# Performance work log

Measured on AMD Instinct MI355X. Metric: run time of the kernel, lower is better.

The kernel has to match this reference:

```python
import jax, jax.numpy as jnp
import numpy as np
import math

DIM = 1024
HEADS = 16
B, N = 2, 2048

POLY = jnp.array([-0.037, 0.481, -2.3, 4.917, -1.791], dtype=jnp.float32)


def adaptive_temperature_softmax(logits):
    # logits: [b, h, n, n]
    original_probs = jax.nn.softmax(logits, axis=-1)
    entropy = jnp.sum(-original_probs * jnp.log(original_probs + 1e-9), axis=-1, keepdims=True)
    e2 = entropy * entropy
    poly_result = POLY[0] * e2 * e2 + POLY[1] * e2 * entropy + POLY[2] * e2 + POLY[3] * entropy + POLY[4]
    beta = jnp.where(entropy > 0.5, jnp.maximum(poly_result, 1.0), 1.0)
    return jax.nn.softmax(logits * beta, axis=-1)


def setup_inputs() -> dict:
    key = jax.random.key(0)
    ks = jax.random.split(key, 5)
    s = 1.0 / math.sqrt(DIM)
    return {
        "x": jax.random.normal(ks[0], (B, N, DIM), dtype=jnp.float32),
        "Wq": jax.random.normal(ks[1], (DIM, DIM), dtype=jnp.float32) * s,
        "Wk": jax.random.normal(ks[2], (DIM, DIM), dtype=jnp.float32) * s,
        "Wv": jax.random.normal(ks[3], (DIM, DIM), dtype=jnp.float32) * s,
        "Wo": jax.random.normal(ks[4], (DIM, DIM), dtype=jnp.float32) * s,
        "bo": jnp.zeros((DIM,), dtype=jnp.float32),
    }


def reference(x, Wq, Wk, Wv, Wo, bo):
    b, n, d = x.shape
    h = HEADS
    hd = d // h
    # torch nn.Linear: y = x @ W.T (+ bias)
    def proj(W):
        t = x @ W.T  # [b, n, d]
        return t.reshape(b, n, h, hd).transpose(0, 2, 1, 3)  # [b, h, n, hd]
    q, k, v = proj(Wq), proj(Wk), proj(Wv)
    sim = jnp.einsum('bhid,bhjd->bhij', q, k) / math.sqrt(hd)
    neg = -jnp.finfo(sim.dtype).max
    causal = jnp.triu(jnp.ones((n, n), dtype=bool), k=1)  # True above diagonal
    sim = jnp.where(causal, neg, sim)
    attn = adaptive_temperature_softmax(sim)
    out = jnp.einsum('bhij,bhjd->bhid', attn, v)
    out = out.transpose(0, 2, 1, 3).reshape(b, n, d)
    return out @ Wo.T + bo
```

## Files before the change

### kernel.cpp

```cpp
#include <hip/hip_runtime.h>
#include <math.h>

#define B_   2
#define N_   2048
#define D_   1024
#define H_   16
#define HD_  64
#define BH_  32
#define M_   4096

typedef __bf16 bf16x8 __attribute__((ext_vector_type(8)));
typedef float  f32x4  __attribute__((ext_vector_type(4)));

__device__ inline unsigned short f2b(float f) {
    unsigned u = __float_as_uint(f);
    u += 0x7FFFu + ((u >> 16) & 1u);
    return (unsigned short)(u >> 16);
}
__device__ inline unsigned short f2b_fast(float f) {
    return (unsigned short)((__float_as_uint(f) + 0x8000u) >> 16);
}

__global__ __launch_bounds__(256)
void cvt_all(const float* __restrict__ x,  const float* __restrict__ wq,
             const float* __restrict__ wk, const float* __restrict__ wv,
             const float* __restrict__ wo, ushort* __restrict__ dst)
{
    int i = blockIdx.x * 256 + threadIdx.x;
    if (i >= 2097152) return;
    int fi = i * 4;
    const float* s; int off;
    if (fi < 4194304) { s = x; off = fi; }
    else {
        int r = fi - 4194304;
        int wsel = r >> 20;
        off = r & 1048575;
        s = (wsel == 0) ? wq : (wsel == 1) ? wk : (wsel == 2) ? wv : wo;
    }
    float4 f = *(const float4*)(s + off);
    ushort4 o;
    o.x = f2b(f.x); o.y = f2b(f.y); o.z = f2b(f.z); o.w = f2b(f.w);
    *(ushort4*)(dst + fi) = o;
}

__global__ __launch_bounds__(256)
void gemm_qkv(const ushort* __restrict__ A,
              const ushort* __restrict__ W0, const ushort* __restrict__ W1,
              const ushort* __restrict__ W2,
              ushort* __restrict__ O0, ushort* __restrict__ O1,
              ushort* __restrict__ O2)
{
    const int z = blockIdx.z;
    const ushort* W = (z == 0) ? W0 : (z == 1) ? W1 : W2;

    __shared__ alignas(16) ushort As[128][40];
    __shared__ alignas(16) ushort Bs[128][40];

    const int t = threadIdx.x;
    const int lane = t & 63, w = t >> 6;
    const int quad = lane >> 4, l15 = lane & 15;
    const int wm = (w >> 1) * 64, wn = (w & 1) * 64;
    const int tileM = blockIdx.x * 128, tileN = blockIdx.y * 128;

    const int r0 = t >> 2, r1 = 64 + (t >> 2);
    const int cg = (t & 3) * 8;
    const ushort* GA0 = A + (size_t)(tileM + r0) * D_ + cg;
    const ushort* GA1 = A + (size_t)(tileM + r1) * D_ + cg;
    const ushort* GB0 = W + (size_t)(tileN + r0) * D_ + cg;
    const ushort* GB1 = W + (size_t)(tileN + r1) * D_ + cg;

    f32x4 acc[4][4];
#pragma unroll
    for (int mt = 0; mt < 4; ++mt)
#pragma unroll
        for (int nt = 0; nt < 4; ++nt) acc[mt][nt] = (f32x4){0.f, 0.f, 0.f, 0.f};

    uint4 pa0 = *(const uint4*)GA0, pa1 = *(const uint4*)GA1;
    uint4 pb0 = *(const uint4*)GB0, pb1 = *(const uint4*)GB1;

    for (int k0 = 0; k0 < D_; k0 += 32) {
        __syncthreads();
        *(uint4*)&As[r0][cg] = pa0;
        *(uint4*)&As[r1][cg] = pa1;
        *(uint4*)&Bs[r0][cg] = pb0;
        *(uint4*)&Bs[r1][cg] = pb1;
        __syncthreads();
        if (k0 + 32 < D_) {
            pa0 = *(const uint4*)(GA0 + k0 + 32);
            pa1 = *(const uint4*)(GA1 + k0 + 32);
            pb0 = *(const uint4*)(GB0 + k0 + 32);
            pb1 = *(const uint4*)(GB1 + k0 + 32);
        }

        bf16x8 af[4], bf[4];
#pragma unroll
        for (int mt = 0; mt < 4; ++mt) af[mt] = *(const bf16x8*)&As[wm + mt * 16 + l15][quad * 8];
#pragma unroll
        for (int nt = 0; nt < 4; ++nt) bf[nt] = *(const bf16x8*)&Bs[wn + nt * 16 + l15][quad * 8];
#pragma unroll
        for (int mt = 0; mt < 4; ++mt)
#pragma unroll
            for (int nt = 0; nt < 4; ++nt)
                acc[mt][nt] = __builtin_amdgcn_mfma_f32_16x16x32_bf16(af[mt], bf[nt], acc[mt][nt], 0, 0, 0);
    }

    ushort* O = (z == 0) ? O0 : (z == 1) ? O1 : O2;
    const float scl = (z == 0) ? 0.18033688f : 1.0f;
#pragma unroll
    for (int mt = 0; mt < 4; ++mt)
#pragma unroll
        for (int nt = 0; nt < 4; ++nt) {
            if (z == 2) {
                int rg0 = tileM + wm + mt * 16 + quad * 4;
                int cgc = tileN + wn + nt * 16 + l15;
                int b = rg0 >> 11, n0 = rg0 & (N_ - 1);
                int h = cgc >> 6, dd = cgc & 63;
                ushort4 o4;
                o4.x = f2b(acc[mt][nt][0]); o4.y = f2b(acc[mt][nt][1]);
                o4.z = f2b(acc[mt][nt][2]); o4.w = f2b(acc[mt][nt][3]);
                *(ushort4*)&O[((size_t)((b * H_ + h) * HD_ + dd)) * N_ + n0] = o4;
            } else {
#pragma unroll
                for (int r = 0; r < 4; ++r) {
                    int rg = tileM + wm + mt * 16 + quad * 4 + r;
                    int cgc = tileN + wn + nt * 16 + l15;
                    int b = rg >> 11, n = rg & (N_ - 1);
                    int h = cgc >> 6, dd = cgc & 63;
                    O[(((size_t)(b * H_ + h)) * N_ + n) * HD_ + dd] = f2b(acc[mt][nt][r] * scl);
                }
            }
        }
}

__global__ __launch_bounds__(256)
void gemm_fin(const ushort* __restrict__ A, const ushort* __restrict__ W,
              const float* __restrict__ bias, float* __restrict__ Of)
{
    __shared__ alignas(16) ushort As[128][40];
    __shared__ alignas(16) ushort Bs[64][40];

    const int t = threadIdx.x;
    const int lane = t & 63, w = t >> 6;
    const int quad = lane >> 4, l15 = lane & 15;
    const int wm = (w >> 1) * 64, wn = (w & 1) * 32;
    const int tileM = blockIdx.x * 128, tileN = blockIdx.y * 64;

    const int r0 = t >> 2, r1 = 64 + (t >> 2);
    const int cg = (t & 3) * 8;
    const ushort* GA0 = A + (size_t)(tileM + r0) * D_ + cg;
    const ushort* GA1 = A + (size_t)(tileM + r1) * D_ + cg;
    const ushort* GB0 = W + (size_t)(tileN + r0) * D_ + cg;

    f32x4 acc[4][2];
#pragma unroll
    for (int mt = 0; mt < 4; ++mt)
#pragma unroll
        for (int nt = 0; nt < 2; ++nt) acc[mt][nt] = (f32x4){0.f, 0.f, 0.f, 0.f};

    uint4 pa0 = *(const uint4*)GA0, pa1 = *(const uint4*)GA1;
    uint4 pb0 = *(const uint4*)GB0;

    for (int k0 = 0; k0 < D_; k0 += 32) {
        __syncthreads();
        *(uint4*)&As[r0][cg] = pa0;
        *(uint4*)&As[r1][cg] = pa1;
        *(uint4*)&Bs[r0 & 63][cg] = pb0;
        __syncthreads();
        if (k0 + 32 < D_) {
            pa0 = *(const uint4*)(GA0 + k0 + 32);
            pa1 = *(const uint4*)(GA1 + k0 + 32);
            pb0 = *(const uint4*)(GB0 + k0 + 32);
        }

        bf16x8 af[4], bf[2];
#pragma unroll
        for (int mt = 0; mt < 4; ++mt) af[mt] = *(const bf16x8*)&As[wm + mt * 16 + l15][quad * 8];
#pragma unroll
        for (int nt = 0; nt < 2; ++nt) bf[nt] = *(const bf16x8*)&Bs[wn + nt * 16 + l15][quad * 8];
#pragma unroll
        for (int mt = 0; mt < 4; ++mt)
#pragma unroll
            for (int nt = 0; nt < 2; ++nt)
                acc[mt][nt] = __builtin_amdgcn_mfma_f32_16x16x32_bf16(af[mt], bf[nt], acc[mt][nt], 0, 0, 0);
    }

#pragma unroll
    for (int mt = 0; mt < 4; ++mt)
#pragma unroll
        for (int nt = 0; nt < 2; ++nt)
#pragma unroll
            for (int r = 0; r < 4; ++r) {
                int rg = tileM + wm + mt * 16 + quad * 4 + r;
                int cgc = tileN + wn + nt * 16 + l15;
                Of[(size_t)rg * D_ + cgc] = acc[mt][nt][r] + bias[cgc];
            }
}

__global__ __launch_bounds__(256)
void attn_mfma(const ushort* __restrict__ Q, const ushort* __restrict__ K,
               const ushort* __restrict__ VT, ushort* __restrict__ AO)
{
    const int bid = blockIdx.x;
    const int qt = 31 - (bid >> 5);
    const int bh = bid & 31;
    const size_t kvbase = (size_t)bh * N_ * HD_;

    __shared__ alignas(16) ushort Ks[128][72];
    __shared__ alignas(16) ushort Vs[64][136];
    __shared__ alignas(16) ushort Ps[4][4][296];

    const int t = threadIdx.x;
    const int lane = t & 63, w = t >> 6;
    const int quad = lane >> 4, l15 = lane & 15;
    const float SH2 = 11.5416913f;
    const float LN2 = 0.69314718f;

    const int skey = t >> 3;
    const int skc  = (t & 7) * 8;
    const ushort* KS = K + kvbase + (size_t)skey * HD_ + skc;
    const int vhd = t >> 4;
    const int vkc = (t & 15) * 8;
    const ushort* VS = VT + kvbase + (size_t)vhd * N_ + vkc;

    const int qrow = w * 16 + quad * 4;
    const int qglob = qt * 64 + qrow;
    const int b = bh >> 4, h = bh & 15;
    const int nCh = (qt + 2) >> 1;

    bf16x8 aq0, aq1;
    {
        const size_t qr = kvbase + (size_t)(qt * 64 + w * 16 + l15) * HD_;
        aq0 = *(const bf16x8*)&Q[qr + quad * 8];
        aq1 = *(const bf16x8*)&Q[qr + 32 + quad * 8];
    }

    float ez[4] = {0.f, 0.f, 0.f, 0.f};
    float sz[4] = {0.f, 0.f, 0.f, 0.f};

    uint4 k0 = *(const uint4*)KS;
    uint4 k1 = *(const uint4*)(KS + 32 * HD_);
    uint4 k2 = *(const uint4*)(KS + 64 * HD_);
    uint4 k3 = *(const uint4*)(KS + 96 * HD_);
    for (int c = 0; c < nCh; ++c) {
        __syncthreads();
        *(uint4*)&Ks[skey][skc]      = k0;
        *(uint4*)&Ks[32 + skey][skc] = k1;
        *(uint4*)&Ks[64 + skey][skc] = k2;
        *(uint4*)&Ks[96 + skey][skc] = k3;
        __syncthreads();
        if (c + 1 < nCh) {
            const ushort* nb = KS + (size_t)(c + 1) * (128 * HD_);
            k0 = *(const uint4*)nb;
            k1 = *(const uint4*)(nb + 32 * HD_);
            k2 = *(const uint4*)(nb + 64 * HD_);
            k3 = *(const uint4*)(nb + 96 * HD_);
        }
        if (c + 1 < nCh) {
#pragma unroll
            for (int nt = 0; nt < 8; ++nt) {
                f32x4 sv = (f32x4){0.f, 0.f, 0.f, 0.f};
                sv = __builtin_amdgcn_mfma_f32_16x16x32_bf16(aq0, *(const bf16x8*)&Ks[nt * 16 + l15][quad * 8], sv, 0, 0, 0);
                sv = __builtin_amdgcn_mfma_f32_16x16x32_bf16(aq1, *(const bf16x8*)&Ks[nt * 16 + l15][32 + quad * 8], sv, 0, 0, 0);
#pragma unroll
                for (int r = 0; r < 4; ++r) {
                    float sh = sv[r] - SH2;
                    float e = __builtin_amdgcn_exp2f(sh);
                    ez[r] += e;
                    sz[r] = fmaf(e, sh, sz[r]);
                }
            }
        } else {
            const int tiles = (((qt + 1) * 64) - c * 128) >> 4;
            const int kb0 = c * 128;
            for (int nt = 0; nt < tiles; ++nt) {
                f32x4 sv = (f32x4){0.f, 0.f, 0.f, 0.f};
                sv = __builtin_amdgcn_mfma_f32_16x16x32_bf16(aq0, *(const bf16x8*)&Ks[nt * 16 + l15][quad * 8], sv, 0, 0, 0);
                sv = __builtin_amdgcn_mfma_f32_16x16x32_bf16(aq1, *(const bf16x8*)&Ks[nt * 16 + l15][32 + quad * 8], sv, 0, 0, 0);
                const int kcol = kb0 + nt * 16 + l15;
#pragma unroll
                for (int r = 0; r < 4; ++r) {
                    float sh = sv[r] - SH2;
                    float e = (kcol <= qglob + r) ? __builtin_amdgcn_exp2f(sh) : 0.f;
                    ez[r] += e;
                    sz[r] = fmaf(e, sh, sz[r]);
                }
            }
        }
    }
#pragma unroll
    for (int r = 0; r < 4; ++r) {
#pragma unroll
        for (int off = 1; off < 16; off <<= 1) {
            ez[r] += __shfl_xor(ez[r], off);
            sz[r] += __shfl_xor(sz[r], off);
        }
    }

    float nbs[4], bl[4];
#pragma unroll
    for (int r = 0; r < 4; ++r) {
        float Z = ez[r];
        float Hh = LN2 * (__builtin_amdgcn_logf(Z) - sz[r] / Z);
        float bb = 1.f;
        if (Hh > 0.5f) {
            float e2 = Hh * Hh;
            float pp = -0.037f * e2 * e2 + 0.481f * e2 * Hh - 2.3f * e2 + 4.917f * Hh - 1.791f;
            bb = fmaxf(pp, 1.f);
        }
        bl[r] = bb;
        nbs[r] = -bb * SH2;
    }

    f32x4 ov[4];
#pragma unroll
    for (int nt = 0; nt < 4; ++nt) ov[nt] = (f32x4){0.f, 0.f, 0.f, 0.f};
    float zp[4] = {0.f, 0.f, 0.f, 0.f};

    k0 = *(const uint4*)KS;
    k1 = *(const uint4*)(KS + 32 * HD_);
    k2 = *(const uint4*)(KS + 64 * HD_);
    k3 = *(const uint4*)(KS + 96 * HD_);
    uint4 v0 = *(const uint4*)VS;
    uint4 v1 = *(const uint4*)(VS + 16 * N_);
    uint4 v2 = *(const uint4*)(VS + 32 * N_);
    uint4 v3 = *(const uint4*)(VS + 48 * N_);
    for (int c = 0; c < nCh; ++c) {
        __syncthreads();
        *(uint4*)&Ks[skey][skc]      = k0;
        *(uint4*)&Ks[32 + skey][skc] = k1;
        *(uint4*)&Ks[64 + skey][skc] = k2;
        *(uint4*)&Ks[96 + skey][skc] = k3;
        *(uint4*)&Vs[vhd][vkc]       = v0;
        *(uint4*)&Vs[16 + vhd][vkc]  = v1;
        *(uint4*)&Vs[32 + vhd][vkc]  = v2;
        *(uint4*)&Vs[48 + vhd][vkc]  = v3;
        __syncthreads();
        if (c + 1 < nCh) {
            const ushort* nk = KS + (size_t)(c + 1) * (128 * HD_);
            k0 = *(const uint4*)nk;
            k1 = *(const uint4*)(nk + 32 * HD_);
            k2 = *(const uint4*)(nk + 64 * HD_);
            k3 = *(const uint4*)(nk + 96 * HD_);
            const ushort* nv = VS + (c + 1) * 128;
            v0 = *(const uint4*)nv;
            v1 = *(const uint4*)(nv + 16 * N_);
            v2 = *(const uint4*)(nv + 32 * N_);
            v3 = *(const uint4*)(nv + 48 * N_);
        }
        const int halves = min(2, (qt + 1) - c * 2);
        for (int hh = 0; hh < halves; ++hh) {
            const bool diag = (c * 2 + hh == qt);

            float wv[4][4];
#pragma unroll
            for (int nt = 0; nt < 4; ++nt) {
                f32x4 sv = (f32x4){0.f, 0.f, 0.f, 0.f};
                sv = __builtin_amdgcn_mfma_f32_16x16x32_bf16(aq0, *(const bf16x8*)&Ks[hh * 64 + nt * 16 + l15][quad * 8], sv, 0, 0, 0);
                sv = __builtin_amdgcn_mfma_f32_16x16x32_bf16(aq1, *(const bf16x8*)&Ks[hh * 64 + nt * 16 + l15][32 + quad * 8], sv, 0, 0, 0);
                const int kcol = nt * 16 + l15;
#pragma unroll
                for (int r = 0; r < 4; ++r) {
                    float e = __builtin_amdgcn_exp2f(fmaf(bl[r], sv[r], nbs[r]));
                    wv[nt][r] = (!diag || (kcol <= qrow + r)) ? e : 0.f;
                }
            }
#pragma unroll
            for (int nt = 0; nt < 4; ++nt)
#pragma unroll
                for (int r = 0; r < 4; ++r)
                    Ps[w][quad][r * 72 + nt * 16 + l15] = f2b_fast(wv[nt][r]);
#pragma unroll
            for (int r = 0; r < 4; ++r)
                zp[r] += (wv[0][r] + wv[1][r]) + (wv[2][r] + wv[3][r]);

            bf16x8 pa0 = *(const bf16x8*)&Ps[w][l15 >> 2][(l15 & 3) * 72 + quad * 8];
            bf16x8 pa1 = *(const bf16x8*)&Ps[w][l15 >> 2][(l15 & 3) * 72 + 32 + quad * 8];
#pragma unroll
            for (int nt = 0; nt < 4; ++nt) {
                ov[nt] = __builtin_amdgcn_mfma_f32_16x16x32_bf16(pa0, *(const bf16x8*)&Vs[nt * 16 + l15][hh * 64 + quad * 8], ov[nt], 0, 0, 0);
                ov[nt] = __builtin_amdgcn_mfma_f32_16x16x32_bf16(pa1, *(const bf16x8*)&Vs[nt * 16 + l15][hh * 64 + 32 + quad * 8], ov[nt], 0, 0, 0);
            }
        }
    }
#pragma unroll
    for (int r = 0; r < 4; ++r)
#pragma unroll
        for (int off = 1; off < 16; off <<= 1) zp[r] += __shfl_xor(zp[r], off);

#pragma unroll
    for (int r = 0; r < 4; ++r) {
        int qg = qt * 64 + w * 16 + quad * 4 + r;
        float inv = 1.f / zp[r];
        size_t rowoff = ((size_t)(b * N_ + qg)) * D_ + h * HD_;
#pragma unroll
        for (int nt = 0; nt < 4; ++nt)
            AO[rowoff + nt * 16 + l15] = f2b(ov[nt][r] * inv);
    }
}

extern "C" void kernel_launch(void* const* d_in, const int* in_sizes, int n_in,
                              void* d_out, int out_size, void* d_ws, size_t ws_size,
                              hipStream_t stream)
{
    const float* x  = (const float*)d_in[0];
    const float* Wq = (const float*)d_in[1];
    const float* Wk = (const float*)d_in[2];
    const float* Wv = (const float*)d_in[3];
    const float* Wo = (const float*)d_in[4];
    const float* bo = (const float*)d_in[5];
    float* out = (float*)d_out;

    ushort* ws  = (ushort*)d_ws;
    ushort* xb  = ws;
    ushort* wqb = ws + 4194304;
    ushort* wkb = ws + 5242880;
    ushort* wvb = ws + 6291456;
    ushort* wob = ws + 7340032;
    ushort* Qb  = ws + 8388608;
    ushort* Kb  = ws + 12582912;
    ushort* Vtb = ws + 16777216;
    ushort* aob = ws + 20971520;

    cvt_all<<<8192, 256, 0, stream>>>(x, Wq, Wk, Wv, Wo, xb);

    gemm_qkv<<<dim3(32, 8, 3), 256, 0, stream>>>(
        xb, wqb, wkb, wvb, Qb, Kb, Vtb);

    attn_mfma<<<dim3(1024), 256, 0, stream>>>(Qb, Kb, Vtb, aob);

    gemm_fin<<<dim3(32, 16), 256, 0, stream>>>(aob, wob, bo, out);
}
```

Measured before the change: 202.0 us.

## Load GEMM tiles directly into LDS and fold softmax shift into MFMA accumulator

The QKV and output-projection GEMMs now use global_load_lds to copy tiles straight from global memory into unpadded shared memory. This replaces the register-staged prefetch and the LDS store step, but it drops the one-step prefetch overlap and the padding that avoided bank conflicts. In the attention kernel, the constant softmax shift is now the initial value of the MFMA accumulator, which removes a subtraction per score. The second pass computes exp2(beta*(s-SH2)) with a multiply instead of an fma with a precomputed offset; the result is mathematically equivalent.

```diff
diff --git a/kernel.cpp b/kernel.cpp
--- a/kernel.cpp
+++ b/kernel.cpp
@@ -11,6 +11,11 @@
 
 typedef __bf16 bf16x8 __attribute__((ext_vector_type(8)));
 typedef float  f32x4  __attribute__((ext_vector_type(4)));
+
+#define AS1_ __attribute__((address_space(1)))
+#define AS3_ __attribute__((address_space(3)))
+#define GLDS16(g, l) __builtin_amdgcn_global_load_lds( \
+    (const AS1_ void*)(g), (AS3_ void*)(l), 16, 0, 0)
 
 __device__ inline unsigned short f2b(float f) {
     unsigned u = __float_as_uint(f);
@@ -53,8 +58,8 @@
     const int z = blockIdx.z;
     const ushort* W = (z == 0) ? W0 : (z == 1) ? W1 : W2;
 
-    __shared__ alignas(16) ushort As[128][40];
-    __shared__ alignas(16) ushort Bs[128][40];
+    __shared__ alignas(16) ushort As[128][32];
+    __shared__ alignas(16) ushort Bs[128][32];
 
     const int t = threadIdx.x;
     const int lane = t & 63, w = t >> 6;
@@ -62,12 +67,9 @@
     const int wm = (w >> 1) * 64, wn = (w & 1) * 64;
     const int tileM = blockIdx.x * 128, tileN = blockIdx.y * 128;
 
-    const int r0 = t >> 2, r1 = 64 + (t >> 2);
-    const int cg = (t & 3) * 8;
-    const ushort* GA0 = A + (size_t)(tileM + r0) * D_ + cg;
-    const ushort* GA1 = A + (size_t)(tileM + r1) * D_ + cg;
-    const ushort* GB0 = W + (size_t)(tileN + r0) * D_ + cg;
-    const ushort* GB1 = W + (size_t)(tileN + r1) * D_ + cg;
+    const int srow = lane >> 2, scol = (lane & 3) * 8;
+    const ushort* GA = A + (size_t)(tileM + w * 16 + srow) * D_ + scol;
+    const ushort* GB = W + (size_t)(tileN + w * 16 + srow) * D_ + scol;
 
     f32x4 acc[4][4];
 #pragma unroll
@@ -75,22 +77,13 @@
 #pragma unroll
         for (int nt = 0; nt < 4; ++nt) acc[mt][nt] = (f32x4){0.f, 0.f, 0.f, 0.f};
 
-    uint4 pa0 = *(const uint4*)GA0, pa1 = *(const uint4*)GA1;
-    uint4 pb0 = *(const uint4*)GB0, pb1 = *(const uint4*)GB1;
-
     for (int k0 = 0; k0 < D_; k0 += 32) {
         __syncthreads();
-        *(uint4*)&As[r0][cg] = pa0;
-        *(uint4*)&As[r1][cg] = pa1;
-        *(uint4*)&Bs[r0][cg] = pb0;
-        *(uint4*)&Bs[r1][cg] = pb1;
-        __syncthreads();
-        if (k0 + 32 < D_) {
-            pa0 = *(const uint4*)(GA0 + k0 + 32);
-            pa1 = *(const uint4*)(GA1 + k0 + 32);
-            pb0 = *(const uint4*)(GB0 + k0 + 32);
-            pb1 = *(const uint4*)(GB1 + k0 + 32);
-        }
+        GLDS16(GA + k0,            &As[w * 16][0]);
+        GLDS16(GA + 64 * D_ + k0,  &As[64 + w * 16][0]);
+        GLDS16(GB + k0,            &Bs[w * 16][0]);
+        GLDS16(GB + 64 * D_ + k0,  &Bs[64 + w * 16][0]);
+        __syncthreads();
 
         bf16x8 af[4], bf[4];
 #pragma unroll
@@ -136,8 +129,8 @@
 void gemm_fin(const ushort* __restrict__ A, const ushort* __restrict__ W,
               const float* __restrict__ bias, float* __restrict__ Of)
 {
-    __shared__ alignas(16) ushort As[128][40];
-    __shared__ alignas(16) ushort Bs[64][40];
+    __shared__ alignas(16) ushort As[128][32];
+    __shared__ alignas(16) ushort Bs[64][32];
 
     const int t = threadIdx.x;
     const int lane = t & 63, w = t >> 6;
@@ -145,11 +138,9 @@
     const int wm = (w >> 1) * 64, wn = (w & 1) * 32;
     const int tileM = blockIdx.x * 128, tileN = blockIdx.y * 64;
 
-    const int r0 = t >> 2, r1 = 64 + (t >> 2);
-    const int cg = (t & 3) * 8;
-    const ushort* GA0 = A + (size_t)(tileM + r0) * D_ + cg;
-    const ushort* GA1 = A + (size_t)(tileM + r1) * D_ + cg;
-    const ushort* GB0 = W + (size_t)(tileN + r0) * D_ + cg;
+    const int srow = lane >> 2, scol = (lane & 3) * 8;
+    const ushort* GA = A + (size_t)(tileM + w * 16 + srow) * D_ + scol;
+    const ushort* GB = W + (size_t)(tileN + w * 16 + srow) * D_ + scol;
 
     f32x4 acc[4][2];
 #pragma unroll
@@ -157,20 +148,12 @@
 #pragma unroll
         for (int nt = 0; nt < 2; ++nt) acc[mt][nt] = (f32x4){0.f, 0.f, 0.f, 0.f};
 
-    uint4 pa0 = *(const uint4*)GA0, pa1 = *(const uint4*)GA1;
-    uint4 pb0 = *(const uint4*)GB0;
-
     for (int k0 = 0; k0 < D_; k0 += 32) {
         __syncthreads();
-        *(uint4*)&As[r0][cg] = pa0;
-        *(uint4*)&As[r1][cg] = pa1;
-        *(uint4*)&Bs[r0 & 63][cg] = pb0;
-        __syncthreads();
-        if (k0 + 32 < D_) {
-            pa0 = *(const uint4*)(GA0 + k0 + 32);
-            pa1 = *(const uint4*)(GA1 + k0 + 32);
-            pb0 = *(const uint4*)(GB0 + k0 + 32);
-        }
+        GLDS16(GA + k0,           &As[w * 16][0]);
+        GLDS16(GA + 64 * D_ + k0, &As[64 + w * 16][0]);
+        GLDS16(GB + k0,           &Bs[w * 16][0]);
+        __syncthreads();
 
         bf16x8 af[4], bf[2];
 #pragma unroll
@@ -258,12 +241,12 @@
         if (c + 1 < nCh) {
 #pragma unroll
             for (int nt = 0; nt < 8; ++nt) {
-                f32x4 sv = (f32x4){0.f, 0.f, 0.f, 0.f};
+                f32x4 sv = (f32x4){-SH2, -SH2, -SH2, -SH2};
                 sv = __builtin_amdgcn_mfma_f32_16x16x32_bf16(aq0, *(const bf16x8*)&Ks[nt * 16 + l15][quad * 8], sv, 0, 0, 0);
                 sv = __builtin_amdgcn_mfma_f32_16x16x32_bf16(aq1, *(const bf16x8*)&Ks[nt * 16 + l15][32 + quad * 8], sv, 0, 0, 0);
 #pragma unroll
                 for (int r = 0; r < 4; ++r) {
-                    float sh = sv[r] - SH2;
+                    float sh = sv[r];
                     float e = __builtin_amdgcn_exp2f(sh);
                     ez[r] += e;
                     sz[r] = fmaf(e, sh, sz[r]);
@@ -273,13 +256,13 @@
             const int tiles = (((qt + 1) * 64) - c * 128) >> 4;
             const int kb0 = c * 128;
             for (int nt = 0; nt < tiles; ++nt) {
-                f32x4 sv = (f32x4){0.f, 0.f, 0.f, 0.f};
+                f32x4 sv = (f32x4){-SH2, -SH2, -SH2, -SH2};
                 sv = __builtin_amdgcn_mfma_f32_16x16x32_bf16(aq0, *(const bf16x8*)&Ks[nt * 16 + l15][quad * 8], sv, 0, 0, 0);
                 sv = __builtin_amdgcn_mfma_f32_16x16x32_bf16(aq1, *(const bf16x8*)&Ks[nt * 16 + l15][32 + quad * 8], sv, 0, 0, 0);
                 const int kcol = kb0 + nt * 16 + l15;
 #pragma unroll
                 for (int r = 0; r < 4; ++r) {
-                    float sh = sv[r] - SH2;
+                    float sh = sv[r];
                     float e = (kcol <= qglob + r) ? __builtin_amdgcn_exp2f(sh) : 0.f;
                     ez[r] += e;
                     sz[r] = fmaf(e, sh, sz[r]);
@@ -296,7 +279,7 @@
         }
     }
 
-    float nbs[4], bl[4];
+    float bl[4];
 #pragma unroll
     for (int r = 0; r < 4; ++r) {
         float Z = ez[r];
@@ -308,7 +291,6 @@
             bb = fmaxf(pp, 1.f);
         }
         bl[r] = bb;
-        nbs[r] = -bb * SH2;
     }
 
     f32x4 ov[4];
@@ -354,13 +336,13 @@
             float wv[4][4];
 #pragma unroll
             for (int nt = 0; nt < 4; ++nt) {
-                f32x4 sv = (f32x4){0.f, 0.f, 0.f, 0.f};
+                f32x4 sv = (f32x4){-SH2, -SH2, -SH2, -SH2};
                 sv = __builtin_amdgcn_mfma_f32_16x16x32_bf16(aq0, *(const bf16x8*)&Ks[hh * 64 + nt * 16 + l15][quad * 8], sv, 0, 0, 0);
                 sv = __builtin_amdgcn_mfma_f32_16x16x32_bf16(aq1, *(const bf16x8*)&Ks[hh * 64 + nt * 16 + l15][32 + quad * 8], sv, 0, 0, 0);
                 const int kcol = nt * 16 + l15;
 #pragma unroll
                 for (int r = 0; r < 4; ++r) {
-                    float e = __builtin_amdgcn_exp2f(fmaf(bl[r], sv[r], nbs[r]));
+                    float e = __builtin_amdgcn_exp2f(bl[r] * sv[r]);
                     wv[nt][r] = (!diag || (kcol <= qrow + r)) ? e : 0.f;
                 }
             }
```

After: 207.7 us. 2.8% more time.
